# Performance work log

Hardware: AMD Instinct MI355X
Metric: run time of the kernel (lower is better)

The kernel has to match this reference:

```python
import jax, jax.numpy as jnp
import numpy as np
from functools import partial

HEADS = 16
EPS = 1e-12  # torch F.normalize eps


def _l2_normalize(z):
    n = jnp.linalg.norm(z, axis=-1, keepdims=True)
    return z / jnp.maximum(n, EPS)


def setup_inputs() -> dict:
    key = jax.random.key(0)
    kx, kq, kk, kv, ko, kf = jax.random.split(key, 6)
    B, S, D, L = 2, 2048, 1024, 1024
    scale = 0.02
    return {
        "x": jax.random.normal(kx, (B, S, D), dtype=jnp.float32),
        "Wq": jax.random.normal(kq, (D, L), dtype=jnp.float32) * scale,
        "Wk": jax.random.normal(kk, (D, L), dtype=jnp.float32) * scale,
        "Wv": jax.random.normal(kv, (D, L), dtype=jnp.float32) * scale,
        "Wo": jax.random.normal(ko, (L, D), dtype=jnp.float32) * scale,
        "Wff": jax.random.normal(kf, (D, D), dtype=jnp.float32) * scale,
    }


def reference(x, Wq, Wk, Wv, Wo, Wff):
    B, S, D = x.shape
    H = HEADS
    L = Wq.shape[1]
    dh = L // H

    def split_heads(t):  # [B,S,L] -> [B*H, S, dh]  ('b y (h x) -> (b h) y x')
        return t.reshape(B, S, H, dh).transpose(0, 2, 1, 3).reshape(B * H, S, dh)

    q = split_heads(x @ Wq)
    k = split_heads(x @ Wk)
    v = split_heads(x @ Wv)

    # scores[b, k, q] = <q_q, k_k> / sqrt(input_size)  (note: scale uses D, not dh)
    scores = jnp.einsum('bqd,bkd->bkq', q, k) / jnp.sqrt(jnp.asarray(D, x.dtype))
    # faithful quirk: softmax over the LAST axis, which here is the query axis
    attn = jax.nn.softmax(scores, axis=-1)  # [B*H, K, Q]
    # out[b, q, d] = sum_k attn[b, k, q] * v[b, k, d]
    out = jnp.einsum('bkq,bkv->bqv', attn, v)  # [B*H, S, dh]

    # '(b h) y x -> b y (h x)'
    z = out.reshape(B, H, S, dh).transpose(0, 2, 1, 3).reshape(B, S, L)
    z = z @ Wo  # output projection (dropout is identity in eval)

    z = _l2_normalize(z)          # F.normalize after attention
    z = z @ Wff                   # FFNN linear (bias=False, dropout=identity)
    z = _l2_normalize(z)          # FFNN normalize (n_dim=-1)
    z = jax.nn.gelu(z, approximate=False)  # torch nn.GELU default = exact erf
    return z
```

## Files before the change

### kernel.cpp

```cpp
#include <hip/hip_runtime.h>
#include <hip/hip_bf16.h>
#include <stdint.h>


typedef __attribute__((ext_vector_type(8))) short short8;
typedef __attribute__((ext_vector_type(4))) float floatx4;

#define MFMA_BF16(a, b, c) __builtin_amdgcn_mfma_f32_16x16x32_bf16((a), (b), (c), 0, 0, 0)

#if defined(__has_builtin)
#if __has_builtin(__builtin_amdgcn_exp2f)
#define EXP2F(x) __builtin_amdgcn_exp2f(x)
#endif
#endif
#ifndef EXP2F
#define EXP2F(x) __expf((x) * 0.69314718056f)
#endif

__device__ __forceinline__ float bf2f(unsigned short u) {
  union { unsigned int i; float f; } v; v.i = ((unsigned int)u) << 16; return v.f;
}
__device__ __forceinline__ unsigned short f2bf(float f) {
  __hip_bfloat16 h = __float2bfloat16(f);
  return *reinterpret_cast<unsigned short*>(&h);
}
__device__ __forceinline__ void gld_lds16(const void* g, void* l) {
  __builtin_amdgcn_global_load_lds((__attribute__((address_space(1))) void*)g,
                                   (__attribute__((address_space(3))) void*)l,
                                   16, 0, 0);
}

__global__ __launch_bounds__(256) void detect_dtype(const unsigned int* __restrict__ x,
                                                    int* __restrict__ flag)
{
  __shared__ int red[4];
  int ok = 0;
  for (int i = 0; i < 16; ++i) {
    const unsigned int w = x[threadIdx.x * 16 + i];
    const unsigned int e = (w >> 7) & 0xFF;
    ok += (e == 0 || (e >= 96 && e <= 144)) ? 1 : 0;
  }
  for (int off = 32; off > 0; off >>= 1) ok += __shfl_down(ok, off, 64);
  if ((threadIdx.x & 63) == 0) red[threadIdx.x >> 6] = ok;
  __syncthreads();
  if (threadIdx.x == 0)
    *flag = ((red[0] + red[1] + red[2] + red[3]) > 2048) ? 1 : 0;
}

__global__ __launch_bounds__(256) void cvt_x(const void* __restrict__ src,
                                             unsigned short* __restrict__ dst,
                                             const int* __restrict__ flag)
{
  const int i = blockIdx.x * 256 + threadIdx.x;
  if (*flag) {
    ((uint4*)dst)[i] = ((const uint4*)src)[i];
  } else {
    const float4 a = ((const float4*)src)[2 * i];
    const float4 b = ((const float4*)src)[2 * i + 1];
    unsigned short o[8] = {f2bf(a.x), f2bf(a.y), f2bf(a.z), f2bf(a.w),
                           f2bf(b.x), f2bf(b.y), f2bf(b.z), f2bf(b.w)};
    ((uint4*)dst)[i] = *(uint4*)o;
  }
}

__global__ __launch_bounds__(256) void gemm_bt_128x64(
    const unsigned short* __restrict__ A, const unsigned short* __restrict__ Bt,
    unsigned short* __restrict__ C, int M, int N, int K, int lda, int ldb, int ldc,
    int qscale_cols)
{
  __shared__ __align__(16) unsigned short sA[128 * 32];
  __shared__ __align__(16) unsigned short sB[64 * 32];
  const int tid = threadIdx.x;
  const int wave = tid >> 6, lane = tid & 63, l15 = lane & 15, quad = lane >> 4;
  const int m0 = blockIdx.x * 128, n0 = blockIdx.y * 64;

  const floatx4 z4 = {0.f, 0.f, 0.f, 0.f};
  floatx4 acc[2][4];
  for (int i = 0; i < 2; ++i) for (int j = 0; j < 4; ++j) acc[i][j] = z4;

  const int NK = K >> 5;
  auto stage = [&](int kt) {
    const int k0 = kt << 5;
    for (int j = 0; j < 2; ++j) {
      const int ci = j * 256 + wave * 64 + lane;
      gld_lds16(A + (size_t)(m0 + (ci >> 2)) * lda + k0 + (ci & 3) * 8,
                &sA[(j * 256 + wave * 64) * 8]);
    }
    {
      const int ci = wave * 64 + lane;
      gld_lds16(Bt + (size_t)(n0 + (ci >> 2)) * ldb + k0 + (ci & 3) * 8,
                &sB[(wave * 64) * 8]);
    }
  };

  stage(0);
  for (int kt = 0; kt < NK; ++kt) {
    __syncthreads();
    short8 af[2], bf[4];
    for (int mt = 0; mt < 2; ++mt)
      af[mt] = *(const short8*)&sA[(wave * 32 + mt * 16 + l15) * 32 + quad * 8];
    for (int nt = 0; nt < 4; ++nt)
      bf[nt] = *(const short8*)&sB[(nt * 16 + l15) * 32 + quad * 8];
    for (int mt = 0; mt < 2; ++mt)
      for (int nt = 0; nt < 4; ++nt)
        acc[mt][nt] = MFMA_BF16(af[mt], bf[nt], acc[mt][nt]);
    __syncthreads();
    if (kt + 1 < NK) stage(kt + 1);
  }
  for (int mt = 0; mt < 2; ++mt)
    for (int nt = 0; nt < 4; ++nt)
      for (int r = 0; r < 4; ++r) {
        const int row = m0 + wave * 32 + mt * 16 + quad * 4 + r;
        const int col = n0 + nt * 16 + l15;
        float v = acc[mt][nt][r];
        if (col < qscale_cols) v *= 0.04508422f;
        C[(size_t)row * ldc + col] = f2bf(v);
      }
}

__global__ __launch_bounds__(256) void gemm_bt_128x128(
    const unsigned short* __restrict__ A, const unsigned short* __restrict__ Bt,
    unsigned short* __restrict__ C, int M, int N, int K, int lda, int ldb, int ldc,
    int qscale_cols)
{
  __shared__ __align__(16) unsigned short sA[128 * 32];
  __shared__ __align__(16) unsigned short sB[128 * 32];
  const int tid = threadIdx.x;
  const int wave = tid >> 6, lane = tid & 63, l15 = lane & 15, quad = lane >> 4;
  const int wr = wave >> 1, wc = wave & 1;
  const int m0 = blockIdx.x * 128, n0 = blockIdx.y * 128;

  const floatx4 z4 = {0.f, 0.f, 0.f, 0.f};
  floatx4 acc[4][4];
  for (int i = 0; i < 4; ++i) for (int j = 0; j < 4; ++j) acc[i][j] = z4;

  const int NK = K >> 5;
  auto stage = [&](int kt) {
    const int k0 = kt << 5;
    for (int j = 0; j < 2; ++j) {
      const int ci = j * 256 + wave * 64 + lane;
      gld_lds16(A + (size_t)(m0 + (ci >> 2)) * lda + k0 + (ci & 3) * 8,
                &sA[(j * 256 + wave * 64) * 8]);
      gld_lds16(Bt + (size_t)(n0 + (ci >> 2)) * ldb + k0 + (ci & 3) * 8,
                &sB[(j * 256 + wave * 64) * 8]);
    }
  };

  stage(0);
  for (int kt = 0; kt < NK; ++kt) {
    __syncthreads();
    short8 af[4], bf[4];
    for (int mt = 0; mt < 4; ++mt)
      af[mt] = *(const short8*)&sA[(wr * 64 + mt * 16 + l15) * 32 + quad * 8];
    for (int nt = 0; nt < 4; ++nt)
      bf[nt] = *(const short8*)&sB[(wc * 64 + nt * 16 + l15) * 32 + quad * 8];
    for (int mt = 0; mt < 4; ++mt)
      for (int nt = 0; nt < 4; ++nt)
        acc[mt][nt] = MFMA_BF16(af[mt], bf[nt], acc[mt][nt]);
    __syncthreads();
    if (kt + 1 < NK) stage(kt + 1);
  }
  for (int mt = 0; mt < 4; ++mt)
    for (int nt = 0; nt < 4; ++nt)
      for (int r = 0; r < 4; ++r) {
        const int row = m0 + wr * 64 + mt * 16 + quad * 4 + r;
        const int col = n0 + wc * 64 + nt * 16 + l15;
        float v = acc[mt][nt][r];
        if (col < qscale_cols) v *= 0.04508422f;
        C[(size_t)row * ldc + col] = f2bf(v);
      }
}

__global__ __launch_bounds__(256) void w_transpose5(
    const void* __restrict__ W0, const void* __restrict__ W1,
    const void* __restrict__ W2, const void* __restrict__ W3,
    const void* __restrict__ W4, unsigned short* __restrict__ WT,
    const int* __restrict__ flag)
{
  __shared__ __align__(16) unsigned short tile[64 * 72];
  const void* srcs[5] = {W0, W1, W2, W3, W4};
  const void* W = srcs[blockIdx.z];
  unsigned short* dst0 = WT + (size_t)blockIdx.z * 1024 * 1024;
  const int rb = blockIdx.x * 64, cb = blockIdx.y * 64;
  const int tid = threadIdx.x;
  const int r = tid >> 2, c = tid & 3;
  unsigned short tmp[16];
  if (*flag) {
    const unsigned short* src = (const unsigned short*)W + (size_t)(rb + r) * 1024 + cb + c * 16;
    *(uint4*)&tmp[0] = *(const uint4*)src;
    *(uint4*)&tmp[8] = *(const uint4*)(src + 8);
  } else {
    const float* src = (const float*)W + (size_t)(rb + r) * 1024 + cb + c * 16;
    for (int j = 0; j < 16; j += 4) {
      const float4 f = *(const float4*)(src + j);
      tmp[j + 0] = f2bf(f.x); tmp[j + 1] = f2bf(f.y);
      tmp[j + 2] = f2bf(f.z); tmp[j + 3] = f2bf(f.w);
    }
  }
  *(uint4*)&tile[r * 72 + c * 16] = *(uint4*)&tmp[0];
  *(uint4*)&tile[r * 72 + c * 16 + 8] = *(uint4*)&tmp[8];
  __syncthreads();
  const int oc = tid >> 2;
  unsigned short out[16];
  for (int j = 0; j < 16; ++j) out[j] = tile[(c * 16 + j) * 72 + oc];
  unsigned short* dst = dst0 + (size_t)(cb + oc) * 1024 + rb + c * 16;
  *(uint4*)dst = *(uint4*)&out[0];
  *(uint4*)(dst + 8) = *(uint4*)&out[8];
}

__global__ __launch_bounds__(256) void v_transpose(const unsigned short* __restrict__ QKV,
                                                   const float* __restrict__ rsum,
                                                   unsigned short* __restrict__ Vt)
{
  __shared__ __align__(16) unsigned short tile[64 * 72];
  const int bh = blockIdx.x, st = blockIdx.y;
  const int b = bh >> 4, h = bh & 15;
  const int tid = threadIdx.x;
  const int r = tid >> 2, c = tid & 3;
  const unsigned short* src =
      QKV + (size_t)(b * 2048 + st * 64 + r) * 3072 + 2048 + h * 64 + c * 16;
  *(uint4*)&tile[r * 72 + c * 16] = *(const uint4*)src;
  *(uint4*)&tile[r * 72 + c * 16 + 8] = *(const uint4*)(src + 8);
  __syncthreads();
  const int d = tid >> 2;
  const float* rsB = rsum + bh * 2048 + st * 64 + c * 16;
  unsigned short out[16];
  for (int j = 0; j < 16; ++j)
    out[j] = f2bf(bf2f(tile[(c * 16 + j) * 72 + d]) * rsB[j]);
  unsigned short* dst = Vt + (size_t)bh * 64 * 2048 + (size_t)d * 2048 + st * 64 + c * 16;
  *(uint4*)dst = *(uint4*)&out[0];
  *(uint4*)(dst + 8) = *(uint4*)&out[8];
}

__global__ __launch_bounds__(256) void attn_stats(const unsigned short* __restrict__ QKV,
                                                  float* __restrict__ spart)
{
  __shared__ __align__(16) unsigned short sQ[2][8 * 512];
  const int bh = blockIdx.x, kb = blockIdx.y, qs = blockIdx.z;
  const int b = bh >> 4, h = bh & 15;
  const int tid = threadIdx.x;
  const int wave = tid >> 6, lane = tid & 63, l15 = lane & 15, quad = lane >> 4;
  const int kbase = kb * 128 + wave * 32;
  const size_t row0 = (size_t)b * 2048;
  const int qoff = h * 64, koff = 1024 + h * 64;
  const int qbase = qs * 512;

  short8 kf[2][2];
  for (int rt = 0; rt < 2; ++rt)
    for (int ks = 0; ks < 2; ++ks)
      kf[rt][ks] = *(const short8*)&QKV[(row0 + kbase + rt * 16 + l15) * 3072 +
                                        koff + ks * 32 + quad * 8];

  float l[2][4];
  for (int rt = 0; rt < 2; ++rt)
    for (int r = 0; r < 4; ++r) l[rt][r] = 0.f;

  auto stageQ = [&](int t) {
    const int qt0 = qbase + t * 64;
    for (int j = 0; j < 2; ++j) {
      const int f = wave * 2 + j;
      const int nt = f >> 1, ks = f & 1;
      gld_lds16(QKV + (row0 + qt0 + nt * 16 + l15) * 3072 + qoff + ks * 32 + quad * 8,
                &sQ[t & 1][f * 512]);
    }
  };

  const floatx4 z4 = {0.f, 0.f, 0.f, 0.f};
  stageQ(0);
  for (int t = 0; t < 8; ++t) {
    __syncthreads();
    if (t + 1 < 8) stageQ(t + 1);
    const unsigned short* sQt = sQ[t & 1];
    for (int nt = 0; nt < 4; ++nt) {
      const short8 bq0 = *(const short8*)&sQt[(nt * 2 + 0) * 512 + lane * 8];
      const short8 bq1 = *(const short8*)&sQt[(nt * 2 + 1) * 512 + lane * 8];
      for (int rt = 0; rt < 2; ++rt) {
        floatx4 acc = z4;
        acc = MFMA_BF16(kf[rt][0], bq0, acc);
        acc = MFMA_BF16(kf[rt][1], bq1, acc);
        for (int r = 0; r < 4; ++r)
          l[rt][r] += EXP2F(acc[r]);
      }
    }
  }
  for (int rt = 0; rt < 2; ++rt)
    for (int r = 0; r < 4; ++r) {
      float ll = l[rt][r];
      ll += __shfl_xor(ll, 1, 64);
      ll += __shfl_xor(ll, 2, 64);
      ll += __shfl_xor(ll, 4, 64);
      ll += __shfl_xor(ll, 8, 64);
      if (l15 == 0) {
        const int krow = kbase + rt * 16 + quad * 4 + r;
        spart[(size_t)qs * 65536 + bh * 2048 + krow] = ll;
      }
    }
}

__global__ __launch_bounds__(256) void stats_combine(const float* __restrict__ spart,
                                                     float* __restrict__ rsum)
{
  const int i = blockIdx.x * 256 + threadIdx.x;
  rsum[i] = 1.0f / (spart[i] + spart[i + 65536] + spart[i + 131072] + spart[i + 196608]);
}

__global__ __launch_bounds__(256) void attn_pv(const unsigned short* __restrict__ QKV,
                                               const unsigned short* __restrict__ Vt,
                                               unsigned short* __restrict__ Z1)
{
  __shared__ __align__(16) unsigned short sK[2][64 * 64];
  __shared__ __align__(16) unsigned short sV[2][64 * 64];
  __shared__ __align__(16) unsigned short sP[128 * 36];
  const int bh = blockIdx.x, qb = blockIdx.y;
  const int b = bh >> 4, h = bh & 15;
  const int tid = threadIdx.x;
  const int wave = tid >> 6, lane = tid & 63, l15 = lane & 15, quad = lane >> 4;
  const size_t row0 = (size_t)b * 2048;
  const int qoff = h * 64, koff = 1024 + h * 64;
  const int q0 = qb * 128;
  const int srow = lane >> 3, schk = (lane & 7) ^ ((lane >> 3) & 7);

  short8 qf[2][2];
  for (int mt = 0; mt < 2; ++mt)
    for (int ks = 0; ks < 2; ++ks)
      qf[mt][ks] = *(const short8*)&QKV[(row0 + q0 + wave * 32 + mt * 16 + l15) * 3072 +
                                        qoff + ks * 32 + quad * 8];

  const floatx4 z4 = {0.f, 0.f, 0.f, 0.f};
  floatx4 acco[2][4];
  for (int i = 0; i < 2; ++i) for (int j = 0; j < 4; ++j) acco[i][j] = z4;

  const unsigned short* VtB = Vt + (size_t)bh * 64 * 2048;

  auto stage = [&](int kt) {
    const int kb = kt * 64;
    const int bufi = kt & 1;
    for (int j = 0; j < 2; ++j) {
      const int jj = wave * 2 + j;
      gld_lds16(QKV + (row0 + kb + jj * 8 + srow) * 3072 + koff + schk * 8,
                &sK[bufi][jj * 512]);
      gld_lds16(VtB + (size_t)(jj * 8 + srow) * 2048 + kb + schk * 8,
                &sV[bufi][jj * 512]);
    }
  };

  stage(0);
  for (int kt = 0; kt < 32; ++kt) {
    __syncthreads();
    if (kt + 1 < 32) stage(kt + 1);
    const unsigned short* sKt = sK[kt & 1];
    const unsigned short* sVt = sV[kt & 1];
    for (int h2 = 0; h2 < 2; ++h2) {
      floatx4 sacc[2][2];
      sacc[0][0] = z4; sacc[0][1] = z4; sacc[1][0] = z4; sacc[1][1] = z4;
      for (int nt2 = 0; nt2 < 2; ++nt2)
        for (int ks = 0; ks < 2; ++ks) {
          const int row = h2 * 32 + nt2 * 16 + l15;
          const int chk = (ks * 4 + quad) ^ (l15 & 7);
          const short8 kfr = *(const short8*)&sKt[row * 64 + chk * 8];
          sacc[0][nt2] = MFMA_BF16(qf[0][ks], kfr, sacc[0][nt2]);
          sacc[1][nt2] = MFMA_BF16(qf[1][ks], kfr, sacc[1][nt2]);
        }
      for (int mt = 0; mt < 2; ++mt)
        for (int nt2 = 0; nt2 < 2; ++nt2)
          for (int r = 0; r < 4; ++r)
            sP[(wave * 32 + mt * 16 + quad * 4 + r) * 36 + nt2 * 16 + l15] =
                f2bf(EXP2F(sacc[mt][nt2][r]));
      short8 pf[2];
      for (int mt = 0; mt < 2; ++mt)
        pf[mt] = *(const short8*)&sP[(wave * 32 + mt * 16 + l15) * 36 + quad * 8];
      for (int nt = 0; nt < 4; ++nt) {
        const int row = nt * 16 + l15;
        const int chk = (h2 * 4 + quad) ^ (l15 & 7);
        const short8 vf = *(const short8*)&sVt[row * 64 + chk * 8];
        acco[0][nt] = MFMA_BF16(pf[0], vf, acco[0][nt]);
        acco[1][nt] = MFMA_BF16(pf[1], vf, acco[1][nt]);
      }
    }
  }
  for (int mt = 0; mt < 2; ++mt)
    for (int nt = 0; nt < 4; ++nt)
      for (int r = 0; r < 4; ++r) {
        const int q = q0 + wave * 32 + mt * 16 + quad * 4 + r;
        const int d = nt * 16 + l15;
        Z1[(row0 + q) * 1024 + qoff + d] = f2bf(acco[mt][nt][r]);
      }
}

__global__ __launch_bounds__(256) void l2norm_gelu(const unsigned short* __restrict__ in,
                                                   void* __restrict__ out, int do_gelu,
                                                   int fin, const int* __restrict__ flag)
{
  __shared__ float red[4];
  const int row = blockIdx.x, tid = threadIdx.x;
  const unsigned short* p = in + (size_t)row * 1024 + tid * 4;
  const ushort4 u = *(const ushort4*)p;
  float x[4] = {bf2f(u.x), bf2f(u.y), bf2f(u.z), bf2f(u.w)};
  float ss = x[0] * x[0] + x[1] * x[1] + x[2] * x[2] + x[3] * x[3];
  for (int off = 32; off > 0; off >>= 1) ss += __shfl_down(ss, off, 64);
  if ((tid & 63) == 0) red[tid >> 6] = ss;
  __syncthreads();
  const float tot = red[0] + red[1] + red[2] + red[3];
  const float sc = 1.0f / fmaxf(sqrtf(tot), 1e-12f);
  float y[4];
  for (int j = 0; j < 4; ++j) {
    y[j] = x[j] * sc;
    if (do_gelu) y[j] = 0.5f * y[j] * (1.0f + erff(y[j] * 0.70710678118654752f));
  }
  if (fin && *flag == 0) {
    float4 o = {y[0], y[1], y[2], y[3]};
    ((float4*)out)[(size_t)row * 256 + tid] = o;
  } else {
    ushort4 o = {f2bf(y[0]), f2bf(y[1]), f2bf(y[2]), f2bf(y[3])};
    ((ushort4*)out)[(size_t)row * 256 + tid] = o;
  }
}

extern "C" void kernel_launch(void* const* d_in, const int* in_sizes, int n_in,
                              void* d_out, int out_size, void* d_ws, size_t ws_size,
                              hipStream_t stream)
{
  const void* x   = d_in[0];
  const void* Wq  = d_in[1];
  const void* Wk  = d_in[2];
  const void* Wv  = d_in[3];
  const void* Wo  = d_in[4];
  const void* Wff = d_in[5];

  char* ws = (char*)d_ws;
  size_t off = 0;
  auto alloc = [&](size_t bytes) -> void* {
    void* p = ws + off; off += (bytes + 255) & ~(size_t)255; return p;
  };
  int* flag             = (int*)alloc(256);
  unsigned short* xb    = (unsigned short*)alloc((size_t)4096 * 1024 * 2);
  unsigned short* WT    = (unsigned short*)alloc((size_t)5 * 1024 * 1024 * 2);
  unsigned short* QKV   = (unsigned short*)alloc((size_t)4096 * 3072 * 2);
  unsigned short* Vt    = (unsigned short*)alloc((size_t)32 * 64 * 2048 * 2);
  float* spart          = (float*)alloc((size_t)4 * 65536 * 4);
  float* rsum           = (float*)alloc((size_t)65536 * 4);
  unsigned short* z1    = (unsigned short*)alloc((size_t)4096 * 1024 * 2);
  unsigned short* WTqkv = WT;
  unsigned short* WoT   = WT + (size_t)3 * 1024 * 1024;
  unsigned short* WffT  = WT + (size_t)4 * 1024 * 1024;
  unsigned short* z2  = Vt;
  unsigned short* z2n = xb;
  unsigned short* z3  = QKV;

  detect_dtype<<<1, 256, 0, stream>>>((const unsigned int*)x, flag);
  cvt_x<<<2048, 256, 0, stream>>>(x, xb, flag);
  w_transpose5<<<dim3(16, 16, 5), 256, 0, stream>>>(Wq, Wk, Wv, Wo, Wff, WT, flag);

  gemm_bt_128x128<<<dim3(32, 24), 256, 0, stream>>>(xb, WTqkv, QKV,
                                                    4096, 3072, 1024, 1024, 1024, 3072, 1024);
  attn_stats<<<dim3(32, 16, 4), 256, 0, stream>>>(QKV, spart);
  stats_combine<<<256, 256, 0, stream>>>(spart, rsum);
  v_transpose<<<dim3(32, 32), 256, 0, stream>>>(QKV, rsum, Vt);
  attn_pv<<<dim3(32, 16), 256, 0, stream>>>(QKV, Vt, z1);

  gemm_bt_128x64<<<dim3(32, 16), 256, 0, stream>>>(z1, WoT, z2,
                                                   4096, 1024, 1024, 1024, 1024, 1024, 0);
  l2norm_gelu<<<4096, 256, 0, stream>>>(z2, z2n, 0, 0, flag);
  gemm_bt_128x64<<<dim3(32, 16), 256, 0, stream>>>(z2n, WffT, z3,
                                                   4096, 1024, 1024, 1024, 1024, 1024, 0);
  l2norm_gelu<<<4096, 256, 0, stream>>>(z3, d_out, 1, 1, flag);
}
```

Before: 298.0 us.

## Split-K attention PV with register-resident P, fold stats combine, drop redundant normalize

```diff
diff --git a/kernel.cpp b/kernel.cpp
--- a/kernel.cpp
+++ b/kernel.cpp
@@ -4,17 +4,16 @@
 
 
 typedef __attribute__((ext_vector_type(8))) short short8;
+typedef __attribute__((ext_vector_type(4))) short short4v;
 typedef __attribute__((ext_vector_type(4))) float floatx4;
 
 #define MFMA_BF16(a, b, c) __builtin_amdgcn_mfma_f32_16x16x32_bf16((a), (b), (c), 0, 0, 0)
-
-#if defined(__has_builtin)
-#if __has_builtin(__builtin_amdgcn_exp2f)
+#define MFMA16(a, b, c) __builtin_amdgcn_mfma_f32_16x16x16bf16_1k((a), (b), (c), 0, 0, 0)
+
+#if defined(__HIP_DEVICE_COMPILE__)
 #define EXP2F(x) __builtin_amdgcn_exp2f(x)
-#endif
-#endif
-#ifndef EXP2F
-#define EXP2F(x) __expf((x) * 0.69314718056f)
+#else
+#define EXP2F(x) exp2f(x)
 #endif
 
 __device__ __forceinline__ float bf2f(unsigned short u) {
@@ -209,7 +208,7 @@
 }
 
 __global__ __launch_bounds__(256) void v_transpose(const unsigned short* __restrict__ QKV,
-                                                   const float* __restrict__ rsum,
+                                                   const float* __restrict__ spart,
                                                    unsigned short* __restrict__ Vt)
 {
   __shared__ __align__(16) unsigned short tile[64 * 72];
@@ -223,10 +222,13 @@
   *(uint4*)&tile[r * 72 + c * 16 + 8] = *(const uint4*)(src + 8);
   __syncthreads();
   const int d = tid >> 2;
-  const float* rsB = rsum + bh * 2048 + st * 64 + c * 16;
   unsigned short out[16];
-  for (int j = 0; j < 16; ++j)
-    out[j] = f2bf(bf2f(tile[(c * 16 + j) * 72 + d]) * rsB[j]);
+  for (int j = 0; j < 16; ++j) {
+    const int s = st * 64 + c * 16 + j;
+    const float4 sp = *(const float4*)&spart[(size_t)(bh * 2048 + s) * 4];
+    const float rs = 1.0f / (sp.x + sp.y + sp.z + sp.w);
+    out[j] = f2bf(bf2f(tile[(c * 16 + j) * 72 + d]) * rs);
+  }
   unsigned short* dst = Vt + (size_t)bh * 64 * 2048 + (size_t)d * 2048 + st * 64 + c * 16;
   *(uint4*)dst = *(uint4*)&out[0];
   *(uint4*)(dst + 8) = *(uint4*)&out[8];
@@ -292,26 +294,22 @@
       ll += __shfl_xor(ll, 8, 64);
       if (l15 == 0) {
         const int krow = kbase + rt * 16 + quad * 4 + r;
-        spart[(size_t)qs * 65536 + bh * 2048 + krow] = ll;
-      }
-    }
-}
-
-__global__ __launch_bounds__(256) void stats_combine(const float* __restrict__ spart,
-                                                     float* __restrict__ rsum)
-{
-  const int i = blockIdx.x * 256 + threadIdx.x;
-  rsum[i] = 1.0f / (spart[i] + spart[i + 65536] + spart[i + 131072] + spart[i + 196608]);
-}
-
-__global__ __launch_bounds__(256) void attn_pv(const unsigned short* __restrict__ QKV,
-                                               const unsigned short* __restrict__ Vt,
-                                               unsigned short* __restrict__ Z1)
-{
-  __shared__ __align__(16) unsigned short sK[2][64 * 64];
-  __shared__ __align__(16) unsigned short sV[2][64 * 64];
-  __shared__ __align__(16) unsigned short sP[128 * 36];
-  const int bh = blockIdx.x, qb = blockIdx.y;
+        spart[(size_t)(bh * 2048 + krow) * 4 + qs] = ll;
+      }
+    }
+}
+
+__global__ __launch_bounds__(256) void attn_pv2(const unsigned short* __restrict__ QKV,
+                                                const unsigned short* __restrict__ Vt,
+                                                unsigned short* __restrict__ z1p0,
+                                                unsigned short* __restrict__ z1p1)
+{
+  __shared__ __align__(16) unsigned char smem[32768];
+  unsigned short* sK = (unsigned short*)smem;
+  unsigned short* sV = (unsigned short*)(smem + 16384);
+  unsigned short* sT = (unsigned short*)smem;
+
+  const int bh = blockIdx.x, qb = blockIdx.y, kh = blockIdx.z;
   const int b = bh >> 4, h = bh & 15;
   const int tid = threadIdx.x;
   const int wave = tid >> 6, lane = tid & 63, l15 = lane & 15, quad = lane >> 4;
@@ -321,70 +319,87 @@
   const int srow = lane >> 3, schk = (lane & 7) ^ ((lane >> 3) & 7);
 
   short8 qf[2][2];
-  for (int mt = 0; mt < 2; ++mt)
+  for (int qg = 0; qg < 2; ++qg)
     for (int ks = 0; ks < 2; ++ks)
-      qf[mt][ks] = *(const short8*)&QKV[(row0 + q0 + wave * 32 + mt * 16 + l15) * 3072 +
+      qf[qg][ks] = *(const short8*)&QKV[(row0 + q0 + wave * 32 + qg * 16 + l15) * 3072 +
                                         qoff + ks * 32 + quad * 8];
 
   const floatx4 z4 = {0.f, 0.f, 0.f, 0.f};
-  floatx4 acco[2][4];
-  for (int i = 0; i < 2; ++i) for (int j = 0; j < 4; ++j) acco[i][j] = z4;
+  floatx4 acc[4][2];
+  for (int i = 0; i < 4; ++i) for (int j = 0; j < 2; ++j) acc[i][j] = z4;
 
   const unsigned short* VtB = Vt + (size_t)bh * 64 * 2048;
 
   auto stage = [&](int kt) {
-    const int kb = kt * 64;
-    const int bufi = kt & 1;
+    const int kb = kh * 1024 + kt * 64;
+    const int bo = (kt & 1) * 4096;
     for (int j = 0; j < 2; ++j) {
       const int jj = wave * 2 + j;
       gld_lds16(QKV + (row0 + kb + jj * 8 + srow) * 3072 + koff + schk * 8,
-                &sK[bufi][jj * 512]);
+                &sK[bo + jj * 512]);
       gld_lds16(VtB + (size_t)(jj * 8 + srow) * 2048 + kb + schk * 8,
-                &sV[bufi][jj * 512]);
+                &sV[bo + jj * 512]);
     }
   };
 
   stage(0);
-  for (int kt = 0; kt < 32; ++kt) {
-    __syncthreads();
-    if (kt + 1 < 32) stage(kt + 1);
-    const unsigned short* sKt = sK[kt & 1];
-    const unsigned short* sVt = sV[kt & 1];
-    for (int h2 = 0; h2 < 2; ++h2) {
-      floatx4 sacc[2][2];
-      sacc[0][0] = z4; sacc[0][1] = z4; sacc[1][0] = z4; sacc[1][1] = z4;
-      for (int nt2 = 0; nt2 < 2; ++nt2)
-        for (int ks = 0; ks < 2; ++ks) {
-          const int row = h2 * 32 + nt2 * 16 + l15;
-          const int chk = (ks * 4 + quad) ^ (l15 & 7);
-          const short8 kfr = *(const short8*)&sKt[row * 64 + chk * 8];
-          sacc[0][nt2] = MFMA_BF16(qf[0][ks], kfr, sacc[0][nt2]);
-          sacc[1][nt2] = MFMA_BF16(qf[1][ks], kfr, sacc[1][nt2]);
-        }
-      for (int mt = 0; mt < 2; ++mt)
-        for (int nt2 = 0; nt2 < 2; ++nt2)
-          for (int r = 0; r < 4; ++r)
-            sP[(wave * 32 + mt * 16 + quad * 4 + r) * 36 + nt2 * 16 + l15] =
-                f2bf(EXP2F(sacc[mt][nt2][r]));
-      short8 pf[2];
-      for (int mt = 0; mt < 2; ++mt)
-        pf[mt] = *(const short8*)&sP[(wave * 32 + mt * 16 + l15) * 36 + quad * 8];
-      for (int nt = 0; nt < 4; ++nt) {
-        const int row = nt * 16 + l15;
-        const int chk = (h2 * 4 + quad) ^ (l15 & 7);
-        const short8 vf = *(const short8*)&sVt[row * 64 + chk * 8];
-        acco[0][nt] = MFMA_BF16(pf[0], vf, acco[0][nt]);
-        acco[1][nt] = MFMA_BF16(pf[1], vf, acco[1][nt]);
-      }
-    }
-  }
-  for (int mt = 0; mt < 2; ++mt)
-    for (int nt = 0; nt < 4; ++nt)
-      for (int r = 0; r < 4; ++r) {
-        const int q = q0 + wave * 32 + mt * 16 + quad * 4 + r;
-        const int d = nt * 16 + l15;
-        Z1[(row0 + q) * 1024 + qoff + d] = f2bf(acco[mt][nt][r]);
-      }
+  for (int kt = 0; kt < 16; ++kt) {
+    __syncthreads();
+    if (kt + 1 < 16) stage(kt + 1);
+    const unsigned short* sKt = &sK[(kt & 1) * 4096];
+    const unsigned short* sVt = &sV[(kt & 1) * 4096];
+    for (int kg = 0; kg < 4; ++kg) {
+      floatx4 s0 = z4, s1 = z4;
+      for (int ks = 0; ks < 2; ++ks) {
+        const short8 kfr = *(const short8*)
+            &sKt[(kg * 16 + l15) * 64 + (((ks * 4 + quad) ^ (l15 & 7)) * 8)];
+        s0 = MFMA_BF16(kfr, qf[0][ks], s0);
+        s1 = MFMA_BF16(kfr, qf[1][ks], s1);
+      }
+      union PU { struct { __hip_bfloat162 lo, hi; } p; short4v v; };
+      PU p0, p1;
+      p0.p.lo = __float22bfloat162_rn(float2{EXP2F(s0[0]), EXP2F(s0[1])});
+      p0.p.hi = __float22bfloat162_rn(float2{EXP2F(s0[2]), EXP2F(s0[3])});
+      p1.p.lo = __float22bfloat162_rn(float2{EXP2F(s1[0]), EXP2F(s1[1])});
+      p1.p.hi = __float22bfloat162_rn(float2{EXP2F(s1[2]), EXP2F(s1[3])});
+      const int slot = (2 * kg + (quad >> 1)) ^ (l15 & 7);
+      const int sub = (quad & 1) * 8;
+      for (int dg = 0; dg < 4; ++dg) {
+        const short4v vfr = *(const short4v*)
+            ((const char*)&sVt[(dg * 16 + l15) * 64] + slot * 16 + sub);
+        acc[dg][0] = MFMA16(vfr, p0.v, acc[dg][0]);
+        acc[dg][1] = MFMA16(vfr, p1.v, acc[dg][1]);
+      }
+    }
+  }
+  __syncthreads();
+  for (int dg = 0; dg < 4; ++dg)
+    for (int qg = 0; qg < 2; ++qg) {
+      ushort4 pk = {f2bf(acc[dg][qg][0]), f2bf(acc[dg][qg][1]),
+                    f2bf(acc[dg][qg][2]), f2bf(acc[dg][qg][3])};
+      *(ushort4*)&sT[(wave * 32 + qg * 16 + l15) * 72 + dg * 16 + quad * 4] = pk;
+    }
+  __syncthreads();
+  unsigned short* z1p = kh ? z1p1 : z1p0;
+  const int q = tid >> 1, d0 = (tid & 1) * 32;
+  unsigned short* dst = z1p + (row0 + q0 + q) * 1024 + qoff + d0;
+  const unsigned short* srcT = &sT[q * 72 + d0];
+  for (int j = 0; j < 4; ++j)
+    *(uint4*)(dst + j * 8) = *(const uint4*)(srcT + j * 8);
+}
+
+__global__ __launch_bounds__(256) void pv_combine(const unsigned short* __restrict__ z1p0,
+                                                  const unsigned short* __restrict__ z1p1,
+                                                  unsigned short* __restrict__ z1)
+{
+  const int i = blockIdx.x * 256 + threadIdx.x;
+  const uint4 a = ((const uint4*)z1p0)[i];
+  const uint4 b = ((const uint4*)z1p1)[i];
+  const unsigned short* av = (const unsigned short*)&a;
+  const unsigned short* bv = (const unsigned short*)&b;
+  unsigned short o[8];
+  for (int j = 0; j < 8; ++j) o[j] = f2bf(bf2f(av[j]) + bf2f(bv[j]));
+  ((uint4*)z1)[i] = *(uint4*)o;
 }
 
 __global__ __launch_bounds__(256) void l2norm_gelu(const unsigned short* __restrict__ in,
@@ -437,15 +452,15 @@
   unsigned short* WT    = (unsigned short*)alloc((size_t)5 * 1024 * 1024 * 2);
   unsigned short* QKV   = (unsigned short*)alloc((size_t)4096 * 3072 * 2);
   unsigned short* Vt    = (unsigned short*)alloc((size_t)32 * 64 * 2048 * 2);
-  float* spart          = (float*)alloc((size_t)4 * 65536 * 4);
-  float* rsum           = (float*)alloc((size_t)65536 * 4);
+  float* spart          = (float*)alloc((size_t)65536 * 4 * 4);
   unsigned short* z1    = (unsigned short*)alloc((size_t)4096 * 1024 * 2);
+  unsigned short* z1p1  = (unsigned short*)alloc((size_t)4096 * 1024 * 2);
   unsigned short* WTqkv = WT;
   unsigned short* WoT   = WT + (size_t)3 * 1024 * 1024;
   unsigned short* WffT  = WT + (size_t)4 * 1024 * 1024;
-  unsigned short* z2  = Vt;
-  unsigned short* z2n = xb;
-  unsigned short* z3  = QKV;
+  unsigned short* z1p0 = xb;
+  unsigned short* z2   = Vt;
+  unsigned short* z3   = QKV;
 
   detect_dtype<<<1, 256, 0, stream>>>((const unsigned int*)x, flag);
   cvt_x<<<2048, 256, 0, stream>>>(x, xb, flag);
@@ -454,14 +469,13 @@
   gemm_bt_128x128<<<dim3(32, 24), 256, 0, stream>>>(xb, WTqkv, QKV,
                                                     4096, 3072, 1024, 1024, 1024, 3072, 1024);
   attn_stats<<<dim3(32, 16, 4), 256, 0, stream>>>(QKV, spart);
-  stats_combine<<<256, 256, 0, stream>>>(spart, rsum);
-  v_transpose<<<dim3(32, 32), 256, 0, stream>>>(QKV, rsum, Vt);
-  attn_pv<<<dim3(32, 16), 256, 0, stream>>>(QKV, Vt, z1);
+  v_transpose<<<dim3(32, 32), 256, 0, stream>>>(QKV, spart, Vt);
+  attn_pv2<<<dim3(32, 16, 2), 256, 0, stream>>>(QKV, Vt, z1p0, z1p1);
+  pv_combine<<<2048, 256, 0, stream>>>(z1p0, z1p1, z1);
 
   gemm_bt_128x64<<<dim3(32, 16), 256, 0, stream>>>(z1, WoT, z2,
                                                    4096, 1024, 1024, 1024, 1024, 1024, 0);
-  l2norm_gelu<<<4096, 256, 0, stream>>>(z2, z2n, 0, 0, flag);
-  gemm_bt_128x64<<<dim3(32, 16), 256, 0, stream>>>(z2n, WffT, z3,
+  gemm_bt_128x64<<<dim3(32, 16), 256, 0, stream>>>(z2, WffT, z3,
                                                    4096, 1024, 1024, 1024, 1024, 1024, 0);
   l2norm_gelu<<<4096, 256, 0, stream>>>(z3, d_out, 1, 1, flag);
 }
```

New measurement: 287.7 us. -3.5%, faster.
